# Kernel optimization log

Hardware: AMD Instinct MI355X
Metric: run time of the kernel (lower is better)

The kernel has to match this reference:

```python
import jax, jax.numpy as jnp
import numpy as np

NUM_HEADS = 16
WINDOW_SIZE = 256  # config.window_size; layer is 'local'


def setup_inputs() -> dict:
    key = jax.random.key(0)
    ks = jax.random.split(key, 8)
    B, S, H = 4, 2048, 1024
    scale = 1.0 / np.sqrt(H)
    return {
        "x": jax.random.normal(ks[0], (B, S, H), dtype=jnp.float32),
        "x_clean": jax.random.normal(ks[1], (B, S, H), dtype=jnp.float32),
        "ablation_mask": jax.random.uniform(ks[2], (B, S, H), dtype=jnp.float32),
        "Wq": jax.random.normal(ks[3], (H, H), dtype=jnp.float32) * scale,
        "Wk": jax.random.normal(ks[4], (H, H), dtype=jnp.float32) * scale,
        "Wv": jax.random.normal(ks[5], (H, H), dtype=jnp.float32) * scale,
        "Wo": jax.random.normal(ks[6], (H, H), dtype=jnp.float32) * scale,
        "bo": jnp.zeros((H,), dtype=jnp.float32),
    }


def reference(x, x_clean, ablation_mask, Wq, Wk, Wv, Wo, bo):
    B, S, H = x.shape
    nh, hd = NUM_HEADS, H // NUM_HEADS

    def proj(inp, W):  # torch Linear: inp @ W.T -> split heads -> [B, nh, S, hd]
        return jnp.einsum('bsh,oh->bso', inp, W).reshape(B, S, nh, hd).transpose(0, 2, 1, 3)

    q = proj(x, Wq)
    k = proj(x_clean, Wk)
    v = proj(x_clean, Wv)

    # NOTE: original applies NO 1/sqrt(head_dim) scaling.
    scores = jnp.einsum('bnsd,bntd->bnst', q, k)  # [B, nh, S, S]

    i = jnp.arange(S)[:, None]
    j = jnp.arange(S)[None, :]
    # local mask: forbid future (j > i) OR too-far past (j <= i - window)
    masked = (j > i) | (j <= i - WINDOW_SIZE)
    scores = jnp.where(masked[None, None, :, :], -jnp.inf, scores)

    attn = jax.nn.softmax(scores, axis=-1)
    context = jnp.einsum('bnst,bntd->bnsd', attn, v)          # [B, nh, S, hd]
    context = context.transpose(0, 2, 1, 3).reshape(B, S, H)   # merge heads
    context = context * ablation_mask
    return jnp.einsum('bsh,oh->bso', context, Wo) + bo
```

## Files before the change

kernel.cpp:

```cpp
#include <hip/hip_runtime.h>
#include <hip/hip_bf16.h>
#include <cstddef>

#define SB 4
#define SS 2048
#define SH 1024
#define NH 16
#define HD 64
#define WIN 256
#define PITCH 40

typedef __attribute__((ext_vector_type(8))) short bf16x8;
typedef __attribute__((ext_vector_type(8))) _Float16 f16x8;
typedef __attribute__((ext_vector_type(2))) __fp16 fp16v2;
typedef __attribute__((ext_vector_type(4))) float f32x4;

static __device__ __forceinline__ ushort2 pk_bf16(float a, float b) {
    __hip_bfloat162 h = __float22bfloat162_rn(make_float2(a, b));
    union { __hip_bfloat162 h2; ushort2 u2; } u;
    u.h2 = h;
    return u.u2;
}
static __device__ __forceinline__ unsigned short pk1(float a) {
    return pk_bf16(a, 0.f).x;
}

__global__ __launch_bounds__(256) void cvt_f16(
    const float* __restrict__ src, _Float16* __restrict__ dst, int n4)
{
    int idx = blockIdx.x * 256 + threadIdx.x;
    if (idx >= n4) return;
    float4 v = ((const float4*)src)[idx];
    union { fp16v2 h[2]; uint2 u; } t;
    t.h[0] = __builtin_amdgcn_cvt_pkrtz(v.x, v.y);
    t.h[1] = __builtin_amdgcn_cvt_pkrtz(v.z, v.w);
    ((uint2*)dst)[idx] = t.u;
}

template<int OUTM>
__global__ __launch_bounds__(256) void gemm3(
    const _Float16* __restrict__ A, const _Float16* __restrict__ W,
    const float* __restrict__ bias, void* __restrict__ C1v,
    int M, int N, int K)
{
    __shared__ __align__(16) unsigned short smem[2 * 128 * PITCH];
    _Float16* Ah = (_Float16*)smem;
    _Float16* Bh = (_Float16*)smem + 128 * PITCH;

    const int tid = threadIdx.x;
    const int m0 = blockIdx.x * 128;
    const int n0 = blockIdx.y * 128;
    const int wave = tid >> 6;
    const int lane = tid & 63;
    const int wm = (wave & 1) * 64;
    const int wn = (wave >> 1) * 64;
    const int lrow = lane & 15;
    const int lk8 = (lane >> 4) * 8;
    const int rq = (lane >> 4) * 4;

    f32x4 acc[4][4];
#pragma unroll
    for (int i = 0; i < 4; ++i)
#pragma unroll
        for (int j = 0; j < 4; ++j)
            acc[i][j] = (f32x4){0.f, 0.f, 0.f, 0.f};

    for (int k0 = 0; k0 < K; k0 += 32) {
        __syncthreads();
#pragma unroll
        for (int u = 0; u < 2; ++u) {
            int slot = u * 256 + tid;
            int row = slot >> 2;
            int k8 = (slot & 3) * 8;
            *(uint4*)&Ah[row * PITCH + k8] =
                *(const uint4*)(A + (size_t)(m0 + row) * K + k0 + k8);
            *(uint4*)&Bh[row * PITCH + k8] =
                *(const uint4*)(W + (size_t)(n0 + row) * K + k0 + k8);
        }
        __syncthreads();

        f16x8 bf[4];
#pragma unroll
        for (int j = 0; j < 4; ++j)
            bf[j] = *(const f16x8*)&Bh[(wn + j * 16 + lrow) * PITCH + lk8];
#pragma unroll
        for (int i = 0; i < 4; ++i) {
            f16x8 af = *(const f16x8*)&Ah[(wm + i * 16 + lrow) * PITCH + lk8];
#pragma unroll
            for (int j = 0; j < 4; ++j)
                acc[i][j] = __builtin_amdgcn_mfma_f32_16x16x32_f16(af, bf[j], acc[i][j], 0, 0, 0);
        }
    }

    if (OUTM == 0) {
        float* C = (float*)C1v;
#pragma unroll
        for (int i = 0; i < 4; ++i) {
            int rbase = m0 + wm + i * 16 + rq;
#pragma unroll
            for (int j = 0; j < 4; ++j) {
                int col = n0 + wn + j * 16 + lrow;
                float badd = bias[col];
#pragma unroll
                for (int r = 0; r < 4; ++r)
                    C[(size_t)(rbase + r) * N + col] = acc[i][j][r] + badd;
            }
        }
    } else if (OUTM == 1) {
        _Float16* C = (_Float16*)C1v;
#pragma unroll
        for (int i = 0; i < 4; ++i) {
            int rbase = m0 + wm + i * 16 + rq;
#pragma unroll
            for (int j = 0; j < 4; ++j) {
                int col = n0 + wn + j * 16 + lrow;
#pragma unroll
                for (int r = 0; r < 4; ++r)
                    C[(size_t)(rbase + r) * N + col] = (_Float16)acc[i][j][r];
            }
        }
    } else {
        unsigned short* Ct = (unsigned short*)C1v;
        unsigned short* T = smem;
#pragma unroll
        for (int p = 0; p < 2; ++p) {
            __syncthreads();
            if (wn == p * 64) {
#pragma unroll
                for (int i = 0; i < 4; ++i) {
                    int mloc = wm + i * 16 + rq;
#pragma unroll
                    for (int j = 0; j < 4; ++j) {
                        int cl = j * 16 + lrow;
                        *(ushort4*)&T[cl * 136 + mloc] = make_ushort4(
                            pk1(acc[i][j][0]), pk1(acc[i][j][1]),
                            pk1(acc[i][j][2]), pk1(acc[i][j][3]));
                    }
                }
            }
            __syncthreads();
#pragma unroll
            for (int u = 0; u < 4; ++u) {
                int slot = u * 256 + tid;
                int cl = slot >> 4;
                int m8 = (slot & 15) * 8;
                *(uint4*)(Ct + (size_t)(n0 + p * 64 + cl) * M + m0 + m8) =
                    *(const uint4*)&T[cl * 136 + m8];
            }
        }
    }
}

__global__ __launch_bounds__(256) void attn_mfma(
    const _Float16* Qg, const _Float16* __restrict__ Kg,
    const unsigned short* __restrict__ Vtg, const float* __restrict__ amask,
    _Float16* ctxg)
{
    __shared__ __align__(16) _Float16 Q_s[128 * 72];
    __shared__ __align__(16) _Float16 K_s[64 * 72];
    __shared__ __align__(16) unsigned short P_s[128 * 72];
    __shared__ __align__(16) unsigned short Vt_s[64 * 72];

    const int t = threadIdx.x;
    const int qb = blockIdx.x, h = blockIdx.y, b = blockIdx.z;
    const int t0 = qb * 128;
    const int wave = t >> 6, lane = t & 63;
    const int lrow = lane & 15;
    const int lk8 = (lane >> 4) * 8;
    const int wq = wave * 32;
    const int rq = (lane >> 4) * 4;

#pragma unroll
    for (int u = 0; u < 4; ++u) {
        int slot = u * 256 + t;
        int row = slot >> 3;
        int d8 = (slot & 7) * 8;
        *(uint4*)&Q_s[row * 72 + d8] =
            *(const uint4*)(Qg + (size_t)(b * SS + t0 + row) * SH + h * HD + d8);
    }

    f32x4 o[2][4];
    float lsum[2][4];
#pragma unroll
    for (int i = 0; i < 2; ++i)
#pragma unroll
        for (int j = 0; j < 4; ++j) o[i][j] = (f32x4){0.f, 0.f, 0.f, 0.f};
#pragma unroll
    for (int i = 0; i < 2; ++i)
#pragma unroll
        for (int r = 0; r < 4; ++r) lsum[i][r] = 0.f;

    int cl = t0 - (WIN - 1);
    cl = cl < 0 ? 0 : cl;
    const int c_lo = cl >> 6;
    const int c_hi = (t0 >> 6) + 1;

    for (int c = c_lo; c <= c_hi; ++c) {
        const int key0 = c * 64;
        __syncthreads();
#pragma unroll
        for (int u = 0; u < 2; ++u) {
            int slot = u * 256 + t;
            int row = slot >> 3;
            int e8 = (slot & 7) * 8;
            *(uint4*)&K_s[row * 72 + e8] =
                *(const uint4*)(Kg + (size_t)(b * SS + key0 + row) * SH + h * HD + e8);
            *(uint4*)&Vt_s[row * 72 + e8] =
                *(const uint4*)(Vtg + (size_t)(h * HD + row) * (SB * SS) + b * SS + key0 + e8);
        }
        __syncthreads();

        f32x4 s[2][4];
#pragma unroll
        for (int i = 0; i < 2; ++i)
#pragma unroll
            for (int j = 0; j < 4; ++j) s[i][j] = (f32x4){0.f, 0.f, 0.f, 0.f};
#pragma unroll
        for (int ki = 0; ki < 2; ++ki) {
            f16x8 ah[2];
#pragma unroll
            for (int i = 0; i < 2; ++i)
                ah[i] = *(const f16x8*)&Q_s[(wq + i * 16 + lrow) * 72 + ki * 32 + lk8];
#pragma unroll
            for (int j = 0; j < 4; ++j) {
                f16x8 bh = *(const f16x8*)&K_s[(j * 16 + lrow) * 72 + ki * 32 + lk8];
#pragma unroll
                for (int i = 0; i < 2; ++i)
                    s[i][j] = __builtin_amdgcn_mfma_f32_16x16x32_f16(ah[i], bh, s[i][j], 0, 0, 0);
            }
        }

#pragma unroll
        for (int i = 0; i < 2; ++i)
#pragma unroll
            for (int j = 0; j < 4; ++j) {
                int jg = key0 + j * 16 + lrow;
#pragma unroll
                for (int r = 0; r < 4; ++r) {
                    int qg = t0 + wq + i * 16 + rq + r;
                    float p = (jg <= qg && jg > qg - WIN) ? __expf(s[i][j][r]) : 0.f;
                    lsum[i][r] += p;
                    P_s[(wq + i * 16 + rq + r) * 72 + j * 16 + lrow] = pk1(p);
                }
            }

#pragma unroll
        for (int ki = 0; ki < 2; ++ki) {
            bf16x8 pf[2];
#pragma unroll
            for (int i = 0; i < 2; ++i)
                pf[i] = *(const bf16x8*)&P_s[(wq + i * 16 + lrow) * 72 + ki * 32 + lk8];
#pragma unroll
            for (int j = 0; j < 4; ++j) {
                bf16x8 vf = *(const bf16x8*)&Vt_s[(j * 16 + lrow) * 72 + ki * 32 + lk8];
#pragma unroll
                for (int i = 0; i < 2; ++i)
                    o[i][j] = __builtin_amdgcn_mfma_f32_16x16x32_bf16(pf[i], vf, o[i][j], 0, 0, 0);
            }
        }
    }

#pragma unroll
    for (int i = 0; i < 2; ++i)
#pragma unroll
        for (int r = 0; r < 4; ++r) {
#pragma unroll
            for (int m = 1; m < 16; m <<= 1)
                lsum[i][r] += __shfl_xor(lsum[i][r], m);
        }

#pragma unroll
    for (int i = 0; i < 2; ++i)
#pragma unroll
        for (int r = 0; r < 4; ++r) {
            float inv = 1.f / lsum[i][r];
            int ql = wq + i * 16 + rq + r;
#pragma unroll
            for (int j = 0; j < 4; ++j) {
                int d = j * 16 + lrow;
                float msk = amask[(size_t)(b * SS + t0 + ql) * SH + h * HD + d];
                Q_s[ql * 72 + d] = (_Float16)(o[i][j][r] * inv * msk);
            }
        }
    __syncthreads();
#pragma unroll
    for (int u = 0; u < 4; ++u) {
        int slot = u * 256 + t;
        int row = slot >> 3;
        int d8 = (slot & 7) * 8;
        *(uint4*)(ctxg + (size_t)(b * SS + t0 + row) * SH + h * HD + d8) =
            *(const uint4*)&Q_s[row * 72 + d8];
    }
}

extern "C" void kernel_launch(void* const* d_in, const int* in_sizes, int n_in,
                              void* d_out, int out_size, void* d_ws, size_t ws_size,
                              hipStream_t stream)
{
    const float* x     = (const float*)d_in[0];
    const float* xc    = (const float*)d_in[1];
    const float* amask = (const float*)d_in[2];
    const float* Wq    = (const float*)d_in[3];
    const float* Wk    = (const float*)d_in[4];
    const float* Wv    = (const float*)d_in[5];
    const float* Wo    = (const float*)d_in[6];
    const float* bo    = (const float*)d_in[7];
    float* out = (float*)d_out;

    const int M = SB * SS;
    const size_t BUF = (size_t)M * SH;
    const size_t WBUF = (size_t)SH * SH;
    _Float16* xh  = (_Float16*)d_ws;
    _Float16* xch = xh + BUF;
    _Float16* Qh  = xch + BUF;
    _Float16* Kh  = Qh + BUF;
    unsigned short* Vt = (unsigned short*)(Kh + BUF);
    _Float16* Wqh = (_Float16*)(Vt + BUF);
    _Float16* Wkh = Wqh + WBUF;
    _Float16* Wvh = Wkh + WBUF;
    _Float16* Woh = Wvh + WBUF;
    _Float16* ctx = Qh;

    const int w4 = SH * SH / 4;
    const int i4 = M * SH / 4;
    hipLaunchKernelGGL(cvt_f16, dim3(i4 / 256), dim3(256), 0, stream, x,  xh,  i4);
    hipLaunchKernelGGL(cvt_f16, dim3(i4 / 256), dim3(256), 0, stream, xc, xch, i4);
    hipLaunchKernelGGL(cvt_f16, dim3(w4 / 256), dim3(256), 0, stream, Wq, Wqh, w4);
    hipLaunchKernelGGL(cvt_f16, dim3(w4 / 256), dim3(256), 0, stream, Wk, Wkh, w4);
    hipLaunchKernelGGL(cvt_f16, dim3(w4 / 256), dim3(256), 0, stream, Wv, Wvh, w4);
    hipLaunchKernelGGL(cvt_f16, dim3(w4 / 256), dim3(256), 0, stream, Wo, Woh, w4);

    dim3 gg(M / 128, SH / 128);
    dim3 gb(256);
    hipLaunchKernelGGL((gemm3<1>), gg, gb, 0, stream, xh,  Wqh, bo, (void*)Qh, M, SH, SH);
    hipLaunchKernelGGL((gemm3<1>), gg, gb, 0, stream, xch, Wkh, bo, (void*)Kh, M, SH, SH);
    hipLaunchKernelGGL((gemm3<2>), gg, gb, 0, stream, xch, Wvh, bo, (void*)Vt, M, SH, SH);

    hipLaunchKernelGGL(attn_mfma, dim3(SS / 128, NH, SB), dim3(256), 0, stream,
                       Qh, Kh, Vt, amask, ctx);

    hipLaunchKernelGGL((gemm3<0>), gg, gb, 0, stream, ctx, Woh, bo, (void*)out, M, SH, SH);
}
```

Before: 319.1 us.

## Use async global-to-LDS loads, keep Q in registers, fuse conversion launches

Replaces the register-staged LDS fills in the GEMMs and attention with global_load_lds direct-to-LDS copies, using unpadded 32-element row layouts. Attention now loads Q fragments straight into registers instead of staging them in shared memory, and writes the masked context directly to global. The six fp32-to-fp16 conversion launches are merged into a single kernel. The unpadded LDS layout may introduce bank conflicts, and the direct ctx stores become narrower scalar writes.

```diff
diff --git a/kernel.cpp b/kernel.cpp
--- a/kernel.cpp
+++ b/kernel.cpp
@@ -8,7 +8,6 @@
 #define NH 16
 #define HD 64
 #define WIN 256
-#define PITCH 40
 
 typedef __attribute__((ext_vector_type(8))) short bf16x8;
 typedef __attribute__((ext_vector_type(8))) _Float16 f16x8;
@@ -25,27 +24,51 @@
     return pk_bf16(a, 0.f).x;
 }
 
-__global__ __launch_bounds__(256) void cvt_f16(
-    const float* __restrict__ src, _Float16* __restrict__ dst, int n4)
+static __device__ __forceinline__ void async16(const void* gptr, void* lptr) {
+    __builtin_amdgcn_global_load_lds(
+        (const __attribute__((address_space(1))) unsigned int*)gptr,
+        (__attribute__((address_space(3))) unsigned int*)lptr, 16, 0, 0);
+}
+
+__global__ __launch_bounds__(256) void cvt_all(
+    const float* __restrict__ x,  const float* __restrict__ xc,
+    const float* __restrict__ Wq, const float* __restrict__ Wk,
+    const float* __restrict__ Wv, const float* __restrict__ Wo,
+    _Float16* __restrict__ xh,  _Float16* __restrict__ xch,
+    _Float16* __restrict__ Wqh, _Float16* __restrict__ Wkh,
+    _Float16* __restrict__ Wvh, _Float16* __restrict__ Woh)
 {
+    const int I4 = SB * SS * SH / 4;
+    const int W4 = SH * SH / 4;
     int idx = blockIdx.x * 256 + threadIdx.x;
-    if (idx >= n4) return;
-    float4 v = ((const float4*)src)[idx];
+    const float* src;
+    _Float16* dst;
+    int off;
+    if (idx < I4) { src = x; dst = xh; off = idx; }
+    else if (idx < 2 * I4) { src = xc; dst = xch; off = idx - I4; }
+    else {
+        int r = idx - 2 * I4;
+        int wi = r >> 18;
+        off = r & (W4 - 1);
+        src = (wi == 0) ? Wq : (wi == 1) ? Wk : (wi == 2) ? Wv : Wo;
+        dst = (wi == 0) ? Wqh : (wi == 1) ? Wkh : (wi == 2) ? Wvh : Woh;
+    }
+    float4 v = ((const float4*)src)[off];
     union { fp16v2 h[2]; uint2 u; } t;
     t.h[0] = __builtin_amdgcn_cvt_pkrtz(v.x, v.y);
     t.h[1] = __builtin_amdgcn_cvt_pkrtz(v.z, v.w);
-    ((uint2*)dst)[idx] = t.u;
+    ((uint2*)dst)[off] = t.u;
 }
 
 template<int OUTM>
-__global__ __launch_bounds__(256) void gemm3(
+__global__ __launch_bounds__(256) void gemm4(
     const _Float16* __restrict__ A, const _Float16* __restrict__ W,
     const float* __restrict__ bias, void* __restrict__ C1v,
     int M, int N, int K)
 {
-    __shared__ __align__(16) unsigned short smem[2 * 128 * PITCH];
+    __shared__ __align__(16) unsigned short smem[(OUTM == 2) ? 8704 : 8192];
     _Float16* Ah = (_Float16*)smem;
-    _Float16* Bh = (_Float16*)smem + 128 * PITCH;
+    _Float16* Bh = (_Float16*)smem + 4096;
 
     const int tid = threadIdx.x;
     const int m0 = blockIdx.x * 128;
@@ -69,23 +92,22 @@
         __syncthreads();
 #pragma unroll
         for (int u = 0; u < 2; ++u) {
-            int slot = u * 256 + tid;
+            int reg = u * 4 + wave;
+            int slot = reg * 64 + lane;
             int row = slot >> 2;
             int k8 = (slot & 3) * 8;
-            *(uint4*)&Ah[row * PITCH + k8] =
-                *(const uint4*)(A + (size_t)(m0 + row) * K + k0 + k8);
-            *(uint4*)&Bh[row * PITCH + k8] =
-                *(const uint4*)(W + (size_t)(n0 + row) * K + k0 + k8);
+            async16(A + (size_t)(m0 + row) * K + k0 + k8, Ah + reg * 512);
+            async16(W + (size_t)(n0 + row) * K + k0 + k8, Bh + reg * 512);
         }
         __syncthreads();
 
         f16x8 bf[4];
 #pragma unroll
         for (int j = 0; j < 4; ++j)
-            bf[j] = *(const f16x8*)&Bh[(wn + j * 16 + lrow) * PITCH + lk8];
+            bf[j] = *(const f16x8*)&Bh[(wn + j * 16 + lrow) * 32 + lk8];
 #pragma unroll
         for (int i = 0; i < 4; ++i) {
-            f16x8 af = *(const f16x8*)&Ah[(wm + i * 16 + lrow) * PITCH + lk8];
+            f16x8 af = *(const f16x8*)&Ah[(wm + i * 16 + lrow) * 32 + lk8];
 #pragma unroll
             for (int j = 0; j < 4; ++j)
                 acc[i][j] = __builtin_amdgcn_mfma_f32_16x16x32_f16(af, bf[j], acc[i][j], 0, 0, 0);
@@ -151,15 +173,14 @@
     }
 }
 
-__global__ __launch_bounds__(256) void attn_mfma(
+__global__ __launch_bounds__(256) void attn2(
     const _Float16* Qg, const _Float16* __restrict__ Kg,
     const unsigned short* __restrict__ Vtg, const float* __restrict__ amask,
     _Float16* ctxg)
 {
-    __shared__ __align__(16) _Float16 Q_s[128 * 72];
-    __shared__ __align__(16) _Float16 K_s[64 * 72];
+    __shared__ __align__(16) _Float16 K_s[2 * 64 * 32];
+    __shared__ __align__(16) unsigned short Vt_s[2 * 64 * 32];
     __shared__ __align__(16) unsigned short P_s[128 * 72];
-    __shared__ __align__(16) unsigned short Vt_s[64 * 72];
 
     const int t = threadIdx.x;
     const int qb = blockIdx.x, h = blockIdx.y, b = blockIdx.z;
@@ -169,15 +190,15 @@
     const int lk8 = (lane >> 4) * 8;
     const int wq = wave * 32;
     const int rq = (lane >> 4) * 4;
-
-#pragma unroll
-    for (int u = 0; u < 4; ++u) {
-        int slot = u * 256 + t;
-        int row = slot >> 3;
-        int d8 = (slot & 7) * 8;
-        *(uint4*)&Q_s[row * 72 + d8] =
-            *(const uint4*)(Qg + (size_t)(b * SS + t0 + row) * SH + h * HD + d8);
-    }
+    const int M = SB * SS;
+
+    f16x8 qf[2][2];
+#pragma unroll
+    for (int i = 0; i < 2; ++i)
+#pragma unroll
+        for (int ki = 0; ki < 2; ++ki)
+            qf[i][ki] = *(const f16x8*)(Qg +
+                (size_t)(b * SS + t0 + wq + i * 16 + lrow) * SH + h * HD + ki * 32 + lk8);
 
     f32x4 o[2][4];
     float lsum[2][4];
@@ -199,14 +220,14 @@
         const int key0 = c * 64;
         __syncthreads();
 #pragma unroll
-        for (int u = 0; u < 2; ++u) {
-            int slot = u * 256 + t;
-            int row = slot >> 3;
-            int e8 = (slot & 7) * 8;
-            *(uint4*)&K_s[row * 72 + e8] =
-                *(const uint4*)(Kg + (size_t)(b * SS + key0 + row) * SH + h * HD + e8);
-            *(uint4*)&Vt_s[row * 72 + e8] =
-                *(const uint4*)(Vtg + (size_t)(h * HD + row) * (SB * SS) + b * SS + key0 + e8);
+        for (int ki = 0; ki < 2; ++ki) {
+            int slot = wave * 64 + lane;
+            int row = slot >> 2;
+            int e8 = (slot & 3) * 8;
+            async16(Kg + (size_t)(b * SS + key0 + row) * SH + h * HD + ki * 32 + e8,
+                    (_Float16*)K_s + ki * 2048 + wave * 512);
+            async16(Vtg + (size_t)(h * HD + row) * M + b * SS + key0 + ki * 32 + e8,
+                    (unsigned short*)Vt_s + ki * 2048 + wave * 512);
         }
         __syncthreads();
 
@@ -217,16 +238,12 @@
             for (int j = 0; j < 4; ++j) s[i][j] = (f32x4){0.f, 0.f, 0.f, 0.f};
 #pragma unroll
         for (int ki = 0; ki < 2; ++ki) {
-            f16x8 ah[2];
-#pragma unroll
-            for (int i = 0; i < 2; ++i)
-                ah[i] = *(const f16x8*)&Q_s[(wq + i * 16 + lrow) * 72 + ki * 32 + lk8];
-#pragma unroll
-            for (int j = 0; j < 4; ++j) {
-                f16x8 bh = *(const f16x8*)&K_s[(j * 16 + lrow) * 72 + ki * 32 + lk8];
+#pragma unroll
+            for (int j = 0; j < 4; ++j) {
+                f16x8 bh = *(const f16x8*)&K_s[ki * 2048 + (j * 16 + lrow) * 32 + lk8];
 #pragma unroll
                 for (int i = 0; i < 2; ++i)
-                    s[i][j] = __builtin_amdgcn_mfma_f32_16x16x32_f16(ah[i], bh, s[i][j], 0, 0, 0);
+                    s[i][j] = __builtin_amdgcn_mfma_f32_16x16x32_f16(qf[i][ki], bh, s[i][j], 0, 0, 0);
             }
         }
 
@@ -252,7 +269,7 @@
                 pf[i] = *(const bf16x8*)&P_s[(wq + i * 16 + lrow) * 72 + ki * 32 + lk8];
 #pragma unroll
             for (int j = 0; j < 4; ++j) {
-                bf16x8 vf = *(const bf16x8*)&Vt_s[(j * 16 + lrow) * 72 + ki * 32 + lk8];
+                bf16x8 vf = *(const bf16x8*)&Vt_s[ki * 2048 + (j * 16 + lrow) * 32 + lk8];
 #pragma unroll
                 for (int i = 0; i < 2; ++i)
                     o[i][j] = __builtin_amdgcn_mfma_f32_16x16x32_bf16(pf[i], vf, o[i][j], 0, 0, 0);
@@ -274,23 +291,14 @@
 #pragma unroll
         for (int r = 0; r < 4; ++r) {
             float inv = 1.f / lsum[i][r];
-            int ql = wq + i * 16 + rq + r;
+            size_t rowb = (size_t)(b * SS + t0 + wq + i * 16 + rq + r) * SH + h * HD;
 #pragma unroll
             for (int j = 0; j < 4; ++j) {
                 int d = j * 16 + lrow;
-                float msk = amask[(size_t)(b * SS + t0 + ql) * SH + h * HD + d];
-                Q_s[ql * 72 + d] = (_Float16)(o[i][j][r] * inv * msk);
-            }
-        }
-    __syncthreads();
-#pragma unroll
-    for (int u = 0; u < 4; ++u) {
-        int slot = u * 256 + t;
-        int row = slot >> 3;
-        int d8 = (slot & 7) * 8;
-        *(uint4*)(ctxg + (size_t)(b * SS + t0 + row) * SH + h * HD + d8) =
-            *(const uint4*)&Q_s[row * 72 + d8];
-    }
+                float msk = amask[rowb + d];
+                ctxg[rowb + d] = (_Float16)(o[i][j][r] * inv * msk);
+            }
+        }
 }
 
 extern "C" void kernel_launch(void* const* d_in, const int* in_sizes, int n_in,
@@ -321,23 +329,18 @@
     _Float16* Woh = Wvh + WBUF;
     _Float16* ctx = Qh;
 
-    const int w4 = SH * SH / 4;
-    const int i4 = M * SH / 4;
-    hipLaunchKernelGGL(cvt_f16, dim3(i4 / 256), dim3(256), 0, stream, x,  xh,  i4);
-    hipLaunchKernelGGL(cvt_f16, dim3(i4 / 256), dim3(256), 0, stream, xc, xch, i4);
-    hipLaunchKernelGGL(cvt_f16, dim3(w4 / 256), dim3(256), 0, stream, Wq, Wqh, w4);
-    hipLaunchKernelGGL(cvt_f16, dim3(w4 / 256), dim3(256), 0, stream, Wk, Wkh, w4);
-    hipLaunchKernelGGL(cvt_f16, dim3(w4 / 256), dim3(256), 0, stream, Wv, Wvh, w4);
-    hipLaunchKernelGGL(cvt_f16, dim3(w4 / 256), dim3(256), 0, stream, Wo, Woh, w4);
+    const int total4 = 2 * (M * SH / 4) + 4 * (SH * SH / 4);
+    hipLaunchKernelGGL(cvt_all, dim3(total4 / 256), dim3(256), 0, stream,
+                       x, xc, Wq, Wk, Wv, Wo, xh, xch, Wqh, Wkh, Wvh, Woh);
 
     dim3 gg(M / 128, SH / 128);
     dim3 gb(256);
-    hipLaunchKernelGGL((gemm3<1>), gg, gb, 0, stream, xh,  Wqh, bo, (void*)Qh, M, SH, SH);
-    hipLaunchKernelGGL((gemm3<1>), gg, gb, 0, stream, xch, Wkh, bo, (void*)Kh, M, SH, SH);
-    hipLaunchKernelGGL((gemm3<2>), gg, gb, 0, stream, xch, Wvh, bo, (void*)Vt, M, SH, SH);
-
-    hipLaunchKernelGGL(attn_mfma, dim3(SS / 128, NH, SB), dim3(256), 0, stream,
+    hipLaunchKernelGGL((gemm4<1>), gg, gb, 0, stream, xh,  Wqh, bo, (void*)Qh, M, SH, SH);
+    hipLaunchKernelGGL((gemm4<1>), gg, gb, 0, stream, xch, Wkh, bo, (void*)Kh, M, SH, SH);
+    hipLaunchKernelGGL((gemm4<2>), gg, gb, 0, stream, xch, Wvh, bo, (void*)Vt, M, SH, SH);
+
+    hipLaunchKernelGGL(attn2, dim3(SS / 128, NH, SB), dim3(256), 0, stream,
                        Qh, Kh, Vt, amask, ctx);
 
-    hipLaunchKernelGGL((gemm3<0>), gg, gb, 0, stream, ctx, Woh, bo, (void*)out, M, SH, SH);
-}
+    hipLaunchKernelGGL((gemm4<0>), gg, gb, 0, stream, ctx, Woh, bo, (void*)out, M, SH, SH);
+}
```

After: 309.7 us. 2.9% less time.
